# Kernel tuning notes

Hardware: AMD Instinct MI355X
Metric: run time of the kernel (lower is better)

The kernel has to match this reference:

```python
import jax, jax.numpy as jnp
import numpy as np

VOCAB = 30000
EMB = 100
HID = 300
SEQ = 200
BATCH = 4096


def setup_inputs() -> dict:
    key = jax.random.key(0)
    ks = jax.random.split(key, 10)
    s_ih = 1.0 / np.sqrt(HID)
    inp = {
        "x": jax.random.randint(ks[0], (SEQ, BATCH), 0, VOCAB, dtype=jnp.int64) if jax.config.jax_enable_x64 else jax.random.randint(ks[0], (SEQ, BATCH), 0, VOCAB, dtype=jnp.int32),
        "emb": jax.random.normal(ks[1], (VOCAB, EMB), dtype=jnp.float32),
        "w_ih": jax.random.uniform(ks[2], (HID, EMB), jnp.float32, -s_ih, s_ih),
        "w_hh": jax.random.uniform(ks[3], (HID, HID), jnp.float32, -s_ih, s_ih),
        "b_ih": jax.random.uniform(ks[4], (HID,), jnp.float32, -s_ih, s_ih),
        "b_hh": jax.random.uniform(ks[5], (HID,), jnp.float32, -s_ih, s_ih),
        "fc1_w": jax.random.uniform(ks[6], (256, HID), jnp.float32, -1/np.sqrt(HID), 1/np.sqrt(HID)),
        "fc1_b": jax.random.uniform(ks[7], (256,), jnp.float32, -1/np.sqrt(HID), 1/np.sqrt(HID)),
        "fc2_w": jax.random.uniform(ks[8], (3, 256), jnp.float32, -1/np.sqrt(256), 1/np.sqrt(256)),
        "fc2_b": jax.random.uniform(ks[9], (3,), jnp.float32, -1/np.sqrt(256), 1/np.sqrt(256)),
    }
    return inp


def reference(x, emb, w_ih, w_hh, b_ih, b_hh, fc1_w, fc1_b, fc2_w, fc2_b):
    # Embedding lookup: [SEQ, BATCH] -> [SEQ, BATCH, EMB]
    xe = emb[x]
    # Precompute input projections for all timesteps (same math, more efficient)
    xp = jnp.einsum('sbe,he->sbh', xe, w_ih) + b_ih + b_hh  # [SEQ, BATCH, HID]
    h0 = jnp.zeros((x.shape[1], HID), dtype=emb.dtype)

    def step(h, xt):
        h = jnp.tanh(xt + h @ w_hh.T)
        return h, None

    ht, _ = jax.lax.scan(step, h0, xp)
    h1 = jax.nn.relu(ht @ fc1_w.T + fc1_b)
    out = h1 @ fc2_w.T + fc2_b
    return out
```

## Files before the change

### kernel.cpp

```cpp
#include <hip/hip_runtime.h>


#define SEQ    200
#define BATCHN 4096
#define EMBD   100
#define HIDN   300

#define KCH   10
#define KCE   4
#define XE0   320
#define BSPAN 448
#define SROW  904
#define ROWS  16

typedef _Float16 half8 __attribute__((ext_vector_type(8)));
typedef float    f32x4 __attribute__((ext_vector_type(4)));

static __device__ __forceinline__ f32x4 f4z() { f32x4 z = {0.f, 0.f, 0.f, 0.f}; return z; }

static __device__ __forceinline__ half8 h8cvt(f32x4 a, f32x4 b) {
  half8 h;
  h[0]=(_Float16)a[0]; h[1]=(_Float16)a[1]; h[2]=(_Float16)a[2]; h[3]=(_Float16)a[3];
  h[4]=(_Float16)b[0]; h[5]=(_Float16)b[1]; h[6]=(_Float16)b[2]; h[7]=(_Float16)b[3];
  return h;
}

static __device__ __forceinline__ half8 loadw(const float* row, int k0, int kmax, bool nv) {
  f32x4 a = (nv && (k0 + 3 < kmax)) ? *(const f32x4*)(row + k0)     : f4z();
  f32x4 b = (nv && (k0 + 7 < kmax)) ? *(const f32x4*)(row + k0 + 4) : f4z();
  return h8cvt(a, b);
}

static __device__ __forceinline__ float tanh_fast(float x) {
  float e = __builtin_amdgcn_exp2f(x * 2.8853900817779268f);
  float r = __builtin_amdgcn_rcpf(e + 1.0f);
  return __builtin_fmaf(-2.0f, r, 1.0f);
}

#define MFMA32(A,B,C) __builtin_amdgcn_mfma_f32_16x16x32_f16((A),(B),(C),0,0,0)

#define STEP_BODY(NT_) do {                                                   \
    _Pragma("unroll")                                                         \
    for (int c = 0; c < KCH; c++) {                                           \
      const half8 a = *(const half8*)(ab + c * 32);                           \
      acc[0] = MFMA32(a, whh[c][0], acc[0]);                                  \
      acc[1] = MFMA32(a, whh[c][1], acc[1]);                                  \
      if (NT_ == 3) acc[2] = MFMA32(a, whh[c][2], acc[2]);                    \
    }                                                                         \
    _Pragma("unroll")                                                         \
    for (int c = 0; c < KCE; c++) {                                           \
      const half8 a = *(const half8*)(ab + XE0 + c * 32);                     \
      acc[0] = MFMA32(a, wih[c][0], acc[0]);                                  \
      acc[1] = MFMA32(a, wih[c][1], acc[1]);                                  \
      if (NT_ == 3) acc[2] = MFMA32(a, wih[c][2], acc[2]);                    \
    }                                                                         \
  } while (0)

__global__ __launch_bounds__(512, 1)
void rnn_fused(const int* __restrict__ x, const float* __restrict__ emb,
               const float* __restrict__ w_ih, const float* __restrict__ w_hh,
               const float* __restrict__ b_ih, const float* __restrict__ b_hh,
               const float* __restrict__ fc1w, const float* __restrict__ fc1b,
               const float* __restrict__ fc2w, const float* __restrict__ fc2b,
               float* __restrict__ out)
{
  __shared__ __align__(16) _Float16 s_lds[ROWS][SROW];
  __shared__ __align__(16) float    h1f[ROWS][257];
  __shared__ int x_lds[SEQ][16];

  const int tid  = (int)threadIdx.x;
  const int lane = tid & 63;
  const int wv   = tid >> 6;
  const int r    = lane & 15;
  const int g    = lane >> 4;
  const int base = (int)blockIdx.x * ROWS;

  const int t0    = (wv < 3) ? wv * 3 : 9 + (wv - 3) * 2;
  const int ntile = (wv < 3) ? 3 : 2;

  for (int i = tid; i < SEQ * 16; i += 512)
    x_lds[i >> 4][i & 15] = x[(i >> 4) * BATCHN + base + (i & 15)];
  for (int i = tid; i < ROWS * SROW; i += 512)
    (&s_lds[0][0])[i] = (_Float16)0.f;

  half8 whh[KCH][3];
  half8 wih[KCE][3];
  float bias[3];
  #pragma unroll
  for (int tt = 0; tt < 3; tt++) {
    const int n = (t0 + tt) * 16 + r;
    const bool nv = (tt < ntile) && (n < HIDN);
    bias[tt] = nv ? (b_ih[n] + b_hh[n]) : 0.f;
    #pragma unroll
    for (int c = 0; c < KCH; c++)
      whh[c][tt] = loadw(w_hh + (long)n * HIDN, c * 32 + 8 * g, HIDN, nv);
    #pragma unroll
    for (int c = 0; c < KCE; c++)
      wih[c][tt] = loadw(w_ih + (long)n * EMBD, c * 32 + 8 * g, EMBD, nv);
  }

  const int gc0 = (wv - 6) * 2;

  __syncthreads();

  if (wv >= 6) {
    const int idx = x_lds[0][r];
    const float* erow = emb + (long)idx * EMBD;
    #pragma unroll
    for (int j = 0; j < 2; j++) {
      const int k0 = (gc0 + j) * 32 + 8 * g;
      f32x4 a = (k0 + 3 < EMBD) ? *(const f32x4*)(erow + k0)     : f4z();
      f32x4 b = (k0 + 7 < EMBD) ? *(const f32x4*)(erow + k0 + 4) : f4z();
      *(half8*)&s_lds[r][XE0 + k0] = h8cvt(a, b);
    }
  }
  __syncthreads();

  const _Float16* a_base = &s_lds[r][8 * g];

  #pragma unroll 2
  for (int t = 0; t < SEQ; t++) {
    const _Float16* ab = a_base + (t & 1) * BSPAN;
    const int nbuf = ((t + 1) & 1) * BSPAN;

    f32x4 xg[2][2];
    if (wv >= 6) {
      const int tn = (t + 1 < SEQ) ? t + 1 : t;
      const int idx = x_lds[tn][r];
      const float* erow = emb + (long)idx * EMBD;
      #pragma unroll
      for (int j = 0; j < 2; j++) {
        const int k0 = (gc0 + j) * 32 + 8 * g;
        xg[j][0] = (k0 + 3 < EMBD) ? *(const f32x4*)(erow + k0)     : f4z();
        xg[j][1] = (k0 + 7 < EMBD) ? *(const f32x4*)(erow + k0 + 4) : f4z();
      }
    }

    f32x4 acc[3];
    #pragma unroll
    for (int tt = 0; tt < 3; tt++) {
      f32x4 v = {bias[tt], bias[tt], bias[tt], bias[tt]};
      acc[tt] = v;
    }

    if (ntile == 3) { STEP_BODY(3); } else { STEP_BODY(2); }

    if (wv >= 6) {
      #pragma unroll
      for (int j = 0; j < 2; j++) {
        const int k0 = (gc0 + j) * 32 + 8 * g;
        *(half8*)&s_lds[r][nbuf + XE0 + k0] = h8cvt(xg[j][0], xg[j][1]);
      }
    }
    #pragma unroll
    for (int tt = 0; tt < 3; tt++) {
      if (tt < ntile) {
        const int n = (t0 + tt) * 16 + r;
        if (n < HIDN) {
          #pragma unroll
          for (int j = 0; j < 4; j++)
            s_lds[4 * g + j][nbuf + n] = (_Float16)tanh_fast(acc[tt][j]);
        }
      }
    }
    __syncthreads();
  }

  {
    const _Float16* abf = a_base + (SEQ & 1) * BSPAN;
    f32x4 acc1[2];
    const int f0 = wv * 2;
    #pragma unroll
    for (int ft = 0; ft < 2; ft++) {
      const float bb = fc1b[(f0 + ft) * 16 + r];
      f32x4 v = {bb, bb, bb, bb};
      acc1[ft] = v;
    }
    #pragma unroll
    for (int c = 0; c < KCH; c++) {
      const half8 a = *(const half8*)(abf + c * 32);
      #pragma unroll
      for (int ft = 0; ft < 2; ft++) {
        const int n = (f0 + ft) * 16 + r;
        const half8 b = loadw(fc1w + (long)n * HIDN, c * 32 + 8 * g, HIDN, true);
        acc1[ft] = MFMA32(a, b, acc1[ft]);
      }
    }
    #pragma unroll
    for (int ft = 0; ft < 2; ft++) {
      const int n = (f0 + ft) * 16 + r;
      #pragma unroll
      for (int j = 0; j < 4; j++) {
        const float v = acc1[ft][j];
        h1f[4 * g + j][n] = v > 0.f ? v : 0.f;
      }
    }
  }
  __syncthreads();

  if (wv == 0 && lane < 48) {
    const int m = lane / 3;
    const int n = lane - 3 * m;
    float s = fc2b[n];
    for (int k = 0; k < 256; k++)
      s = __builtin_fmaf(h1f[m][k], fc2w[n * 256 + k], s);
    out[(base + m) * 3 + n] = s;
  }
}

extern "C" void kernel_launch(void* const* d_in, const int* in_sizes, int n_in,
                              void* d_out, int out_size, void* d_ws, size_t ws_size,
                              hipStream_t stream) {
  (void)in_sizes; (void)n_in; (void)d_ws; (void)ws_size; (void)out_size;
  const int*   x   = (const int*)d_in[0];
  const float* emb = (const float*)d_in[1];
  const float* wih = (const float*)d_in[2];
  const float* whh = (const float*)d_in[3];
  const float* bih = (const float*)d_in[4];
  const float* bhh = (const float*)d_in[5];
  const float* f1w = (const float*)d_in[6];
  const float* f1b = (const float*)d_in[7];
  const float* f2w = (const float*)d_in[8];
  const float* f2b = (const float*)d_in[9];
  rnn_fused<<<BATCHN / ROWS, 512, 0, stream>>>(
      x, emb, wih, whh, bih, bhh, f1w, f1b, f2w, f2b, (float*)d_out);
}
```

Before: 333.7 us.

## Split recurrent K dimension across wave pairs with LDS partial-sum reduction

Result: slower. 428.9 us (+28.5%).

```diff
diff --git a/kernel.cpp b/kernel.cpp
--- a/kernel.cpp
+++ b/kernel.cpp
@@ -6,12 +6,14 @@
 #define EMBD   100
 #define HIDN   300
 
-#define KCH   10
-#define KCE   4
+#define KCHF  10
+#define KCHH  5
+#define KCEH  2
 #define XE0   320
 #define BSPAN 448
 #define SROW  904
 #define ROWS  16
+#define NT    5
 
 typedef _Float16 half8 __attribute__((ext_vector_type(8)));
 typedef float    f32x4 __attribute__((ext_vector_type(4)));
@@ -41,18 +43,22 @@
 
 #define STEP_BODY(NT_) do {                                                   \
     _Pragma("unroll")                                                         \
-    for (int c = 0; c < KCH; c++) {                                           \
-      const half8 a = *(const half8*)(ab + c * 32);                           \
+    for (int c = 0; c < KCHH; c++) {                                          \
+      const half8 a = *(const half8*)(ab + (kh0 + c) * 32);                   \
       acc[0] = MFMA32(a, whh[c][0], acc[0]);                                  \
       acc[1] = MFMA32(a, whh[c][1], acc[1]);                                  \
-      if (NT_ == 3) acc[2] = MFMA32(a, whh[c][2], acc[2]);                    \
+      acc[2] = MFMA32(a, whh[c][2], acc[2]);                                  \
+      acc[3] = MFMA32(a, whh[c][3], acc[3]);                                  \
+      if (NT_ == 5) acc[4] = MFMA32(a, whh[c][4], acc[4]);                    \
     }                                                                         \
     _Pragma("unroll")                                                         \
-    for (int c = 0; c < KCE; c++) {                                           \
-      const half8 a = *(const half8*)(ab + XE0 + c * 32);                     \
+    for (int c = 0; c < KCEH; c++) {                                          \
+      const half8 a = *(const half8*)(ab + XE0 + (ke0 + c) * 32);             \
       acc[0] = MFMA32(a, wih[c][0], acc[0]);                                  \
       acc[1] = MFMA32(a, wih[c][1], acc[1]);                                  \
-      if (NT_ == 3) acc[2] = MFMA32(a, wih[c][2], acc[2]);                    \
+      acc[2] = MFMA32(a, wih[c][2], acc[2]);                                  \
+      acc[3] = MFMA32(a, wih[c][3], acc[3]);                                  \
+      if (NT_ == 5) acc[4] = MFMA32(a, wih[c][4], acc[4]);                    \
     }                                                                         \
   } while (0)
 
@@ -65,6 +71,7 @@
                float* __restrict__ out)
 {
   __shared__ __align__(16) _Float16 s_lds[ROWS][SROW];
+  __shared__ __align__(16) float    pbuf[19][16][16];
   __shared__ __align__(16) float    h1f[ROWS][257];
   __shared__ int x_lds[SEQ][16];
 
@@ -75,44 +82,46 @@
   const int g    = lane >> 4;
   const int base = (int)blockIdx.x * ROWS;
 
-  const int t0    = (wv < 3) ? wv * 3 : 9 + (wv - 3) * 2;
-  const int ntile = (wv < 3) ? 3 : 2;
+  const int p = wv & 3;
+  const int q = wv >> 2;
+  const int t0    = p * NT;
+  const int ntile = (p < 3) ? NT : 4;
+  const int kh0   = q * KCHH;
+  const int ke0   = q * KCEH;
 
   for (int i = tid; i < SEQ * 16; i += 512)
     x_lds[i >> 4][i & 15] = x[(i >> 4) * BATCHN + base + (i & 15)];
   for (int i = tid; i < ROWS * SROW; i += 512)
     (&s_lds[0][0])[i] = (_Float16)0.f;
 
-  half8 whh[KCH][3];
-  half8 wih[KCE][3];
-  float bias[3];
+  half8 whh[KCHH][NT];
+  half8 wih[KCEH][NT];
+  float bias[NT];
   #pragma unroll
-  for (int tt = 0; tt < 3; tt++) {
+  for (int tt = 0; tt < NT; tt++) {
     const int n = (t0 + tt) * 16 + r;
     const bool nv = (tt < ntile) && (n < HIDN);
     bias[tt] = nv ? (b_ih[n] + b_hh[n]) : 0.f;
     #pragma unroll
-    for (int c = 0; c < KCH; c++)
-      whh[c][tt] = loadw(w_hh + (long)n * HIDN, c * 32 + 8 * g, HIDN, nv);
-    #pragma unroll
-    for (int c = 0; c < KCE; c++)
-      wih[c][tt] = loadw(w_ih + (long)n * EMBD, c * 32 + 8 * g, EMBD, nv);
-  }
-
-  const int gc0 = (wv - 6) * 2;
+    for (int c = 0; c < KCHH; c++)
+      whh[c][tt] = loadw(w_hh + (long)n * HIDN, (kh0 + c) * 32 + 8 * g, HIDN, nv);
+    #pragma unroll
+    for (int c = 0; c < KCEH; c++)
+      wih[c][tt] = loadw(w_ih + (long)n * EMBD, (ke0 + c) * 32 + 8 * g, EMBD, nv);
+  }
+
+  const int rr = lane & 15;
+  const int sl = p * 4 + (lane >> 4);
+  const int k0 = 8 * sl;
 
   __syncthreads();
 
-  if (wv >= 6) {
-    const int idx = x_lds[0][r];
+  if (q == 0) {
+    const int idx = x_lds[0][rr];
     const float* erow = emb + (long)idx * EMBD;
-    #pragma unroll
-    for (int j = 0; j < 2; j++) {
-      const int k0 = (gc0 + j) * 32 + 8 * g;
-      f32x4 a = (k0 + 3 < EMBD) ? *(const f32x4*)(erow + k0)     : f4z();
-      f32x4 b = (k0 + 7 < EMBD) ? *(const f32x4*)(erow + k0 + 4) : f4z();
-      *(half8*)&s_lds[r][XE0 + k0] = h8cvt(a, b);
-    }
+    f32x4 a = (k0 + 3 < EMBD) ? *(const f32x4*)(erow + k0)     : f4z();
+    f32x4 b = (k0 + 7 < EMBD) ? *(const f32x4*)(erow + k0 + 4) : f4z();
+    *(half8*)&s_lds[rr][XE0 + k0] = h8cvt(a, b);
   }
   __syncthreads();
 
@@ -123,43 +132,45 @@
     const _Float16* ab = a_base + (t & 1) * BSPAN;
     const int nbuf = ((t + 1) & 1) * BSPAN;
 
-    f32x4 xg[2][2];
-    if (wv >= 6) {
+    f32x4 xga, xgb;
+    if (q == 0) {
       const int tn = (t + 1 < SEQ) ? t + 1 : t;
-      const int idx = x_lds[tn][r];
+      const int idx = x_lds[tn][rr];
       const float* erow = emb + (long)idx * EMBD;
-      #pragma unroll
-      for (int j = 0; j < 2; j++) {
-        const int k0 = (gc0 + j) * 32 + 8 * g;
-        xg[j][0] = (k0 + 3 < EMBD) ? *(const f32x4*)(erow + k0)     : f4z();
-        xg[j][1] = (k0 + 7 < EMBD) ? *(const f32x4*)(erow + k0 + 4) : f4z();
-      }
-    }
-
-    f32x4 acc[3];
-    #pragma unroll
-    for (int tt = 0; tt < 3; tt++) {
-      f32x4 v = {bias[tt], bias[tt], bias[tt], bias[tt]};
+      xga = (k0 + 3 < EMBD) ? *(const f32x4*)(erow + k0)     : f4z();
+      xgb = (k0 + 7 < EMBD) ? *(const f32x4*)(erow + k0 + 4) : f4z();
+    }
+
+    f32x4 acc[NT];
+    #pragma unroll
+    for (int tt = 0; tt < NT; tt++) {
+      const float bb = q ? bias[tt] : 0.f;
+      f32x4 v = {bb, bb, bb, bb};
       acc[tt] = v;
     }
 
-    if (ntile == 3) { STEP_BODY(3); } else { STEP_BODY(2); }
-
-    if (wv >= 6) {
-      #pragma unroll
-      for (int j = 0; j < 2; j++) {
-        const int k0 = (gc0 + j) * 32 + 8 * g;
-        *(half8*)&s_lds[r][nbuf + XE0 + k0] = h8cvt(xg[j][0], xg[j][1]);
-      }
-    }
-    #pragma unroll
-    for (int tt = 0; tt < 3; tt++) {
-      if (tt < ntile) {
-        const int n = (t0 + tt) * 16 + r;
-        if (n < HIDN) {
-          #pragma unroll
-          for (int j = 0; j < 4; j++)
-            s_lds[4 * g + j][nbuf + n] = (_Float16)tanh_fast(acc[tt][j]);
+    if (ntile == 5) { STEP_BODY(5); } else { STEP_BODY(4); }
+
+    if (q == 0) {
+      #pragma unroll
+      for (int tt = 0; tt < NT; tt++)
+        if (tt < ntile)
+          *(f32x4*)&pbuf[t0 + tt][r][4 * g] = acc[tt];
+      *(half8*)&s_lds[rr][nbuf + XE0 + k0] = h8cvt(xga, xgb);
+    }
+    __syncthreads();
+
+    if (q == 1) {
+      #pragma unroll
+      for (int tt = 0; tt < NT; tt++) {
+        if (tt < ntile) {
+          const int n = (t0 + tt) * 16 + r;
+          if (n < HIDN) {
+            const f32x4 part = *(const f32x4*)&pbuf[t0 + tt][r][4 * g];
+            #pragma unroll
+            for (int j = 0; j < 4; j++)
+              s_lds[4 * g + j][nbuf + n] = (_Float16)tanh_fast(acc[tt][j] + part[j]);
+          }
         }
       }
     }
@@ -177,7 +188,7 @@
       acc1[ft] = v;
     }
     #pragma unroll
-    for (int c = 0; c < KCH; c++) {
+    for (int c = 0; c < KCHF; c++) {
       const half8 a = *(const half8*)(abf + c * 32);
       #pragma unroll
       for (int ft = 0; ft < 2; ft++) {
```
